# Performance work log

Hardware: AMD Instinct MI355X
Metric: run time of the kernel (lower is better)

The kernel has to match this reference:

```python
import jax, jax.numpy as jnp
import numpy as np

DIM = 256
EPS = 1e-5

def setup_inputs() -> dict:
    key = jax.random.key(0)
    ks = jax.random.split(key, 10)
    B, S, D = 8, 4096, DIM
    sc = 1.0 / np.sqrt(D)
    return {
        "supervised_embedding": jax.random.normal(ks[0], (B, S, D), jnp.float32),
        "transformer_embedding": jax.random.normal(ks[1], (B, S, D), jnp.float32),
        "Wq": jax.random.normal(ks[2], (D, D), jnp.float32) * sc,
        "bq": jnp.zeros((D,), jnp.float32),
        "Wk": jax.random.normal(ks[3], (D, D), jnp.float32) * sc,
        "bk": jnp.zeros((D,), jnp.float32),
        "Wv": jax.random.normal(ks[4], (D, D), jnp.float32) * sc,
        "bv": jnp.zeros((D,), jnp.float32),
        "gamma": jnp.ones((D,), jnp.float32),
        "beta": jnp.zeros((D,), jnp.float32),
    }

def _layernorm(x, gamma, beta):
    mu = jnp.mean(x, axis=-1, keepdims=True)
    var = jnp.mean(jnp.square(x - mu), axis=-1, keepdims=True)
    return (x - mu) * jax.lax.rsqrt(var + EPS) * gamma + beta

def reference(supervised_embedding, transformer_embedding, Wq, bq, Wk, bk, Wv, bv, gamma, beta):
    # torch Linear: y = x @ W.T + b
    q = transformer_embedding @ Wq.T + bq          # [B,S,D]
    k = supervised_embedding @ Wk.T + bk           # [B,S,D]
    v = supervised_embedding @ Wv.T + bv           # [B,S,D]
    scale = 1.0 / jnp.sqrt(jnp.asarray(q.shape[-1], q.dtype))
    scores = jnp.einsum('bqd,bkd->bqk', q, k) * scale  # [B,S,S]
    w = jax.nn.softmax(scores, axis=-1)
    combined = jnp.einsum('bqk,bkd->bqd', w, v)    # [B,S,D]
    out = _layernorm(combined + transformer_embedding, gamma, beta)
    return jnp.squeeze(out, axis=1) if out.shape[1] == 1 else out
```

## Files before the change

### kernel.cpp

```cpp
#include <hip/hip_runtime.h>
#include <hip/hip_bf16.h>

typedef short s16x8 __attribute__((ext_vector_type(8)));
typedef unsigned short u16x4 __attribute__((ext_vector_type(4)));
typedef float f32x4 __attribute__((ext_vector_type(4)));
typedef unsigned short u16;

#define DEV static __device__ __forceinline__

#if __has_builtin(__builtin_amdgcn_exp2f)
#define EXP2F(x) __builtin_amdgcn_exp2f(x)
#else
#define EXP2F(x) exp2f(x)
#endif

constexpr int D    = 256;
constexpr int SEQ  = 4096;
constexpr int NB   = 8;
constexpr int NTOK = NB * SEQ;
constexpr size_t N_EMB = (size_t)NTOK * D;
constexpr size_t N_W   = (size_t)D * D;
constexpr float SM_C = 0.09016844005556021f;
constexpr float SMAX = 128.0f;

DEV u16 f2bf(float f){ unsigned v; __builtin_memcpy(&v,&f,4); v += 0x7fffu + ((v>>16)&1u); return (u16)(v>>16); }

DEV float rsum16(float v){
  v += __shfl_xor(v,1); v += __shfl_xor(v,2);
  v += __shfl_xor(v,4); v += __shfl_xor(v,8);
  return v;
}

DEV void gl2lds16(const u16* g, void* lds){
  __builtin_amdgcn_global_load_lds(
      (const __attribute__((address_space(1))) void*)g,
      (__attribute__((address_space(3))) void*)lds, 16, 0, 0);
}
DEV void lgkm_barrier(){
  __builtin_amdgcn_s_waitcnt(0xC07F);
  __builtin_amdgcn_s_barrier();
}

__global__ __launch_bounds__(256)
void cvt_all(const float* __restrict__ TE, const float* __restrict__ SE,
             const float* __restrict__ Wq, const float* __restrict__ Wk,
             const float* __restrict__ Wv, u16* __restrict__ dst)
{
  const size_t total4 = (2*N_EMB + 3*N_W) / 4;
  for (size_t i = (size_t)blockIdx.x*256 + threadIdx.x; i < total4;
       i += (size_t)gridDim.x*256) {
    size_t e = i*4;
    const float* s;
    if      (e < N_EMB)            s = TE + e;
    else if (e < 2*N_EMB)          s = SE + (e - N_EMB);
    else if (e < 2*N_EMB + N_W)    s = Wq + (e - 2*N_EMB);
    else if (e < 2*N_EMB + 2*N_W)  s = Wk + (e - 2*N_EMB - N_W);
    else                           s = Wv + (e - 2*N_EMB - 2*N_W);
    f32x4 v = *(const f32x4*)s;
    u16x4 o;
#pragma unroll
    for (int j = 0; j < 4; j++) o[j] = f2bf(v[j]);
    *(u16x4*)(dst + e) = o;
  }
}

__global__ __launch_bounds__(256, 3)
void qkv_proj(const u16* __restrict__ TEb, const u16* __restrict__ SEb,
              const u16* __restrict__ Wqb, const float* __restrict__ bq,
              const u16* __restrict__ Wkb, const float* __restrict__ bk,
              const u16* __restrict__ Wvb, const float* __restrict__ bv,
              u16* __restrict__ Qb, u16* __restrict__ Kb, u16* __restrict__ Vt)
{
  __shared__ __align__(16) char wlds[32768];
  const int tid  = threadIdx.x;
  const int lane = tid & 63, wv = tid >> 6;
  const int li   = lane & 15, grp = lane >> 4;
  const int mode  = blockIdx.y >> 2;
  const int strip = blockIdx.y & 3;
  const int o0    = strip * 64;
  const int tbase = blockIdx.x * 512;

  const u16*   X    = (mode == 0) ? TEb : SEb;
  const u16*   W    = (mode == 0) ? Wqb : (mode == 1) ? Wkb : Wvb;
  const float* bias = (mode == 0) ? bq  : (mode == 1) ? bk  : bv;

#pragma unroll
  for (int c = 0; c < 8; c++) {
    int g = tid + 256*c;
    int r = g >> 5, jj = g & 31;
    *(s16x8*)(wlds + r*512 + 16*(jj ^ (r & 7))) =
        *(const s16x8*)(W + (size_t)(o0 + r)*D + jj*8);
  }
  __syncthreads();

#pragma unroll 1
  for (int tt = 0; tt < 2; tt++) {
    const int base = tbase + tt*256 + wv*64;
    f32x4 acc[16];
#pragma unroll
    for (int i = 0; i < 16; i++) acc[i] = (f32x4){0.f,0.f,0.f,0.f};

    if (mode < 2) {
#pragma unroll
      for (int ks = 0; ks < 8; ks++) {
        s16x8 a[4], bw[4];
#pragma unroll
        for (int mt = 0; mt < 4; mt++)
          a[mt] = *(const s16x8*)(X + (size_t)(base + 16*mt + li)*D + ks*32 + grp*8);
#pragma unroll
        for (int nt = 0; nt < 4; nt++) {
          int r = 16*nt + li;
          bw[nt] = *(const s16x8*)(wlds + r*512 + 16*((4*ks + grp) ^ (r & 7)));
        }
#pragma unroll
        for (int mt = 0; mt < 4; mt++)
#pragma unroll
          for (int nt = 0; nt < 4; nt++)
            acc[mt*4+nt] = __builtin_amdgcn_mfma_f32_16x16x32_bf16(a[mt], bw[nt], acc[mt*4+nt], 0,0,0);
      }
      u16* Y = (mode == 0) ? Qb : Kb;
#pragma unroll
      for (int nt = 0; nt < 4; nt++) {
        int col = o0 + 16*nt + li;
        float bb = bias[col];
#pragma unroll
        for (int mt = 0; mt < 4; mt++)
#pragma unroll
          for (int r = 0; r < 4; r++)
            Y[(size_t)(base + 16*mt + grp*4 + r)*D + col] = f2bf(acc[mt*4+nt][r] + bb);
      }
    } else {
#pragma unroll
      for (int ks = 0; ks < 8; ks++) {
        s16x8 aw[4], bx[4];
#pragma unroll
        for (int at = 0; at < 4; at++) {
          int r = 16*at + li;
          aw[at] = *(const s16x8*)(wlds + r*512 + 16*((4*ks + grp) ^ (r & 7)));
        }
#pragma unroll
        for (int bt = 0; bt < 4; bt++)
          bx[bt] = *(const s16x8*)(X + (size_t)(base + 16*bt + li)*D + ks*32 + grp*8);
#pragma unroll
        for (int at = 0; at < 4; at++)
#pragma unroll
          for (int bt = 0; bt < 4; bt++)
            acc[at*4+bt] = __builtin_amdgcn_mfma_f32_16x16x32_bf16(aw[at], bx[bt], acc[at*4+bt], 0,0,0);
      }
      const int b = base >> 12, s0 = base & (SEQ - 1);
#pragma unroll
      for (int at = 0; at < 4; at++) {
#pragma unroll
        for (int r = 0; r < 4; r++) {
          int o = o0 + 16*at + grp*4 + r;
          float bb = bias[o];
          u16* yrow = Vt + ((size_t)b*D + o)*SEQ + s0;
#pragma unroll
          for (int bt = 0; bt < 4; bt++)
            yrow[16*bt + li] = f2bf(acc[at*4+bt][r] + bb);
        }
      }
    }
  }
}

constexpr int KB0   = 0;
constexpr int KB1   = 16384;
constexpr int P_OFF = 32768;
constexpr int PSTR  = 36;
constexpr int L_OFF = 37376;
constexpr int G_OFF = 37632;
constexpr int BE_OFF= 38656;
constexpr int LDS_SZ= 39680;
constexpr int NIT   = SEQ / 32;

__global__ __launch_bounds__(256, 3)
void attn_ln(const u16* __restrict__ Qb, const u16* __restrict__ Kb,
             const u16* __restrict__ Vt, const float* __restrict__ TE,
             const float* __restrict__ gamma, const float* __restrict__ beta,
             float* __restrict__ out)
{
  __shared__ __align__(16) char smem[LDS_SZ];
  const int tid  = threadIdx.x;
  const int lane = tid & 63, wv = tid >> 6;
  const int li   = lane & 15, grp = lane >> 4;
  const int b  = blockIdx.x & 7;
  const int q0 = (blockIdx.x >> 3) * 64;

  float* gam = (float*)(smem + G_OFF);
  float* bet = (float*)(smem + BE_OFF);
  gam[tid] = gamma[tid];
  bet[tid] = beta[tid];

  const u16* Kbase = Kb + (size_t)b * SEQ * D;
  const u16* Vbase = Vt + (size_t)b * D * SEQ;

  const u16* qrow = Qb + ((size_t)b*SEQ + q0 + 16*wv + li)*D + grp*8;
  s16x8 qf[8];
#pragma unroll
  for (int ks = 0; ks < 8; ks++) qf[ks] = *(const s16x8*)(qrow + ks*32);

  int soff[4];
#pragma unroll
  for (int c = 0; c < 4; c++) {
    int u = wv*4 + c;
    int r = 2*u + (lane >> 5);
    soff[c] = r*256 + (((lane & 31) ^ (r & 7)) * 8);
  }
  int voff[4];
#pragma unroll
  for (int nt = 0; nt < 4; nt++) voff[nt] = (64*wv + 16*nt + li)*SEQ + grp*8;

#pragma unroll
  for (int c = 0; c < 4; c++)
    gl2lds16(Kbase + soff[c], smem + KB0 + (wv*4 + c)*1024);

  f32x4 oacc[16];
#pragma unroll
  for (int i = 0; i < 16; i++) oacc[i] = (f32x4){0.f,0.f,0.f,0.f};
  float l_r[4] = {0.f,0.f,0.f,0.f};

  u16* Pl = (u16*)(smem + P_OFF);

  for (int it = 0; it < NIT; it++) {
    const int k0 = it * 32;
    __syncthreads();

    {
      const u16* Kt = Kbase + (size_t)((it+1 < NIT) ? (k0+32) : k0) * D;
      char* kbn = smem + ((it & 1) ? KB0 : KB1);
#pragma unroll
      for (int c = 0; c < 4; c++)
        gl2lds16(Kt + soff[c], kbn + (wv*4 + c)*1024);
    }
    s16x8 vf[4];
#pragma unroll
    for (int nt = 0; nt < 4; nt++)
      vf[nt] = *(const s16x8*)(Vbase + voff[nt] + k0);

    const char* kb = smem + ((it & 1) ? KB1 : KB0);
    f32x4 sa0 = {0.f,0.f,0.f,0.f}, sa1 = {0.f,0.f,0.f,0.f};
    {
      const int r0 = li, r1 = li + 16;
      const char* kp0 = kb + r0*512;
      const char* kp1 = kb + r1*512;
#pragma unroll
      for (int ks = 0; ks < 8; ks++) {
        s16x8 k0f = *(const s16x8*)(kp0 + 16*((4*ks + grp) ^ (r0 & 7)));
        sa0 = __builtin_amdgcn_mfma_f32_16x16x32_bf16(qf[ks], k0f, sa0, 0,0,0);
        s16x8 k1f = *(const s16x8*)(kp1 + 16*((4*ks + grp) ^ (r1 & 7)));
        sa1 = __builtin_amdgcn_mfma_f32_16x16x32_bf16(qf[ks], k1f, sa1, 0,0,0);
      }
    }

#pragma unroll
    for (int r = 0; r < 4; r++) {
      float p0 = EXP2F((sa0[r] - SMAX) * SM_C);
      float p1 = EXP2F((sa1[r] - SMAX) * SM_C);
      l_r[r] += p0 + p1;
      int row = 16*wv + grp*4 + r;
      Pl[row*PSTR + li]      = f2bf(p0);
      Pl[row*PSTR + li + 16] = f2bf(p1);
    }
    lgkm_barrier();

#pragma unroll
    for (int mt = 0; mt < 4; mt++) {
      s16x8 pf = *(const s16x8*)(smem + P_OFF + ((16*mt + li)*PSTR + grp*8)*2);
#pragma unroll
      for (int nt = 0; nt < 4; nt++)
        oacc[mt*4+nt] = __builtin_amdgcn_mfma_f32_16x16x32_bf16(pf, vf[nt], oacc[mt*4+nt], 0,0,0);
    }
  }

  float* l_lds = (float*)(smem + L_OFF);
  {
#pragma unroll
    for (int r = 0; r < 4; r++) {
      float lt = rsum16(l_r[r]);
      if (li == 0) l_lds[16*wv + grp*4 + r] = lt;
    }
  }
  __syncthreads();

  const float* Tg = TE + ((size_t)b*SEQ + q0) * D;
  float s1[4][4], s2[4][4];
#pragma unroll
  for (int mt = 0; mt < 4; mt++) {
#pragma unroll
    for (int r = 0; r < 4; r++) {
      int row = 16*mt + grp*4 + r;
      float linv = 1.0f / l_lds[row];
      float ps = 0.f, pq = 0.f;
#pragma unroll
      for (int nt = 0; nt < 4; nt++) {
        int d_ = 64*wv + 16*nt + li;
        float x = oacc[mt*4+nt][r] * linv + Tg[(size_t)row*D + d_];
        oacc[mt*4+nt][r] = x;
        ps += x; pq += x * x;
      }
      s1[mt][r] = rsum16(ps);
      s2[mt][r] = rsum16(pq);
    }
  }
  float* part1 = (float*)(smem + P_OFF);
  float* part2 = (float*)(smem + P_OFF + 1024);
  if (li == 0) {
#pragma unroll
    for (int mt = 0; mt < 4; mt++)
#pragma unroll
      for (int r = 0; r < 4; r++) {
        int row = 16*mt + grp*4 + r;
        part1[row*4 + wv] = s1[mt][r];
        part2[row*4 + wv] = s2[mt][r];
      }
  }
  __syncthreads();
#pragma unroll
  for (int mt = 0; mt < 4; mt++) {
#pragma unroll
    for (int r = 0; r < 4; r++) {
      int row = 16*mt + grp*4 + r;
      float su = part1[row*4+0] + part1[row*4+1] + part1[row*4+2] + part1[row*4+3];
      float sq = part2[row*4+0] + part2[row*4+1] + part2[row*4+2] + part2[row*4+3];
      float mu  = su * (1.0f/256.0f);
      float var = sq * (1.0f/256.0f) - mu*mu;
      float rstd = rsqrtf(var + 1e-5f);
      float* orow = out + ((size_t)b*SEQ + q0 + row) * D;
#pragma unroll
      for (int nt = 0; nt < 4; nt++) {
        int d_ = 64*wv + 16*nt + li;
        orow[d_] = (oacc[mt*4+nt][r] - mu) * rstd * gam[d_] + bet[d_];
      }
    }
  }
}

extern "C" void kernel_launch(void* const* d_in, const int* in_sizes, int n_in,
                              void* d_out, int out_size, void* d_ws, size_t ws_size,
                              hipStream_t stream)
{
  (void)in_sizes; (void)n_in; (void)out_size; (void)ws_size;
  const float* SE = (const float*)d_in[0];
  const float* TE = (const float*)d_in[1];
  const float* Wq = (const float*)d_in[2];
  const float* bq = (const float*)d_in[3];
  const float* Wk = (const float*)d_in[4];
  const float* bk = (const float*)d_in[5];
  const float* Wv = (const float*)d_in[6];
  const float* bv = (const float*)d_in[7];
  const float* gm = (const float*)d_in[8];
  const float* bt = (const float*)d_in[9];

  u16* Qb  = (u16*)d_ws;
  u16* Kb  = Qb + N_EMB;
  u16* Vtr = Kb + N_EMB;
  u16* CVT = Vtr + N_EMB;
  u16* TEb = CVT;
  u16* SEb = TEb + N_EMB;
  u16* Wqb = SEb + N_EMB;
  u16* Wkb = Wqb + N_W;
  u16* Wvb = Wkb + N_W;

  cvt_all<<<2048, 256, 0, stream>>>(TE, SE, Wq, Wk, Wv, CVT);
  qkv_proj<<<dim3(NTOK/512, 12), 256, 0, stream>>>(TEb, SEb, Wqb, bq, Wkb, bk, Wvb, bv, Qb, Kb, Vtr);
  attn_ln<<<dim3((SEQ/64) * NB), 256, 0, stream>>>(Qb, Kb, Vtr, TE, gm, bt, (float*)d_out);
}
```

Baseline: 340.1 us.

## Split attention over key halves and combine with a separate layernorm kernel

```diff
diff --git a/kernel.cpp b/kernel.cpp
--- a/kernel.cpp
+++ b/kernel.cpp
@@ -23,6 +23,7 @@
 constexpr float SM_C = 0.09016844005556021f;
 constexpr float SMAX = 128.0f;
 
+DEV float bf2f(u16 u){ unsigned v = ((unsigned)u) << 16; float f; __builtin_memcpy(&f,&v,4); return f; }
 DEV u16 f2bf(float f){ unsigned v; __builtin_memcpy(&v,&f,4); v += 0x7fffu + ((v>>16)&1u); return (u16)(v>>16); }
 
 DEV float rsum16(float v){
@@ -64,7 +65,7 @@
   }
 }
 
-__global__ __launch_bounds__(256, 3)
+__global__ __launch_bounds__(256, 2)
 void qkv_proj(const u16* __restrict__ TEb, const u16* __restrict__ SEb,
               const u16* __restrict__ Wqb, const float* __restrict__ bq,
               const u16* __restrict__ Wkb, const float* __restrict__ bk,
@@ -100,13 +101,27 @@
 #pragma unroll
     for (int i = 0; i < 16; i++) acc[i] = (f32x4){0.f,0.f,0.f,0.f};
 
+    const u16* xr[4];
+#pragma unroll
+    for (int mt = 0; mt < 4; mt++)
+      xr[mt] = X + (size_t)(base + 16*mt + li)*D + grp*8;
+
+    s16x8 xa[4], xb[4];
+#pragma unroll
+    for (int mt = 0; mt < 4; mt++) xa[mt] = *(const s16x8*)(xr[mt]);
+
     if (mode < 2) {
+      u16* Y = (mode == 0) ? Qb : Kb;
 #pragma unroll
       for (int ks = 0; ks < 8; ks++) {
-        s16x8 a[4], bw[4];
-#pragma unroll
-        for (int mt = 0; mt < 4; mt++)
-          a[mt] = *(const s16x8*)(X + (size_t)(base + 16*mt + li)*D + ks*32 + grp*8);
+        s16x8* cu = (ks & 1) ? xb : xa;
+        s16x8* nx = (ks & 1) ? xa : xb;
+        if (ks < 7) {
+#pragma unroll
+          for (int mt = 0; mt < 4; mt++)
+            nx[mt] = *(const s16x8*)(xr[mt] + (ks+1)*32);
+        }
+        s16x8 bw[4];
 #pragma unroll
         for (int nt = 0; nt < 4; nt++) {
           int r = 16*nt + li;
@@ -116,9 +131,8 @@
         for (int mt = 0; mt < 4; mt++)
 #pragma unroll
           for (int nt = 0; nt < 4; nt++)
-            acc[mt*4+nt] = __builtin_amdgcn_mfma_f32_16x16x32_bf16(a[mt], bw[nt], acc[mt*4+nt], 0,0,0);
-      }
-      u16* Y = (mode == 0) ? Qb : Kb;
+            acc[mt*4+nt] = __builtin_amdgcn_mfma_f32_16x16x32_bf16(cu[mt], bw[nt], acc[mt*4+nt], 0,0,0);
+      }
 #pragma unroll
       for (int nt = 0; nt < 4; nt++) {
         int col = o0 + 16*nt + li;
@@ -132,20 +146,24 @@
     } else {
 #pragma unroll
       for (int ks = 0; ks < 8; ks++) {
-        s16x8 aw[4], bx[4];
+        s16x8* cu = (ks & 1) ? xb : xa;
+        s16x8* nx = (ks & 1) ? xa : xb;
+        if (ks < 7) {
+#pragma unroll
+          for (int bt = 0; bt < 4; bt++)
+            nx[bt] = *(const s16x8*)(xr[bt] + (ks+1)*32);
+        }
+        s16x8 aw[4];
 #pragma unroll
         for (int at = 0; at < 4; at++) {
           int r = 16*at + li;
           aw[at] = *(const s16x8*)(wlds + r*512 + 16*((4*ks + grp) ^ (r & 7)));
         }
 #pragma unroll
-        for (int bt = 0; bt < 4; bt++)
-          bx[bt] = *(const s16x8*)(X + (size_t)(base + 16*bt + li)*D + ks*32 + grp*8);
-#pragma unroll
         for (int at = 0; at < 4; at++)
 #pragma unroll
           for (int bt = 0; bt < 4; bt++)
-            acc[at*4+bt] = __builtin_amdgcn_mfma_f32_16x16x32_bf16(aw[at], bx[bt], acc[at*4+bt], 0,0,0);
+            acc[at*4+bt] = __builtin_amdgcn_mfma_f32_16x16x32_bf16(aw[at], cu[bt], acc[at*4+bt], 0,0,0);
       }
       const int b = base >> 12, s0 = base & (SEQ - 1);
 #pragma unroll
@@ -168,32 +186,25 @@
 constexpr int KB1   = 16384;
 constexpr int P_OFF = 32768;
 constexpr int PSTR  = 36;
-constexpr int L_OFF = 37376;
-constexpr int G_OFF = 37632;
-constexpr int BE_OFF= 38656;
-constexpr int LDS_SZ= 39680;
-constexpr int NIT   = SEQ / 32;
-
-__global__ __launch_bounds__(256, 3)
-void attn_ln(const u16* __restrict__ Qb, const u16* __restrict__ Kb,
-             const u16* __restrict__ Vt, const float* __restrict__ TE,
-             const float* __restrict__ gamma, const float* __restrict__ beta,
-             float* __restrict__ out)
-{
-  __shared__ __align__(16) char smem[LDS_SZ];
+constexpr int LDS_A = 37376;
+constexpr int NIT   = 64;
+
+__global__ __launch_bounds__(256, 2)
+void attn_fa(const u16* __restrict__ Qb, const u16* __restrict__ Kb,
+             const u16* __restrict__ Vt,
+             u16* __restrict__ O0, u16* __restrict__ O1, float* __restrict__ lsum)
+{
+  __shared__ __align__(16) char smem[LDS_A];
   const int tid  = threadIdx.x;
   const int lane = tid & 63, wv = tid >> 6;
   const int li   = lane & 15, grp = lane >> 4;
   const int b  = blockIdx.x & 7;
-  const int q0 = (blockIdx.x >> 3) * 64;
-
-  float* gam = (float*)(smem + G_OFF);
-  float* bet = (float*)(smem + BE_OFF);
-  gam[tid] = gamma[tid];
-  bet[tid] = beta[tid];
-
-  const u16* Kbase = Kb + (size_t)b * SEQ * D;
-  const u16* Vbase = Vt + (size_t)b * D * SEQ;
+  const int h  = (blockIdx.x >> 3) & 1;
+  const int q0 = (blockIdx.x >> 4) * 64;
+  u16* Op = h ? O1 : O0;
+
+  const u16* Kbase = Kb + ((size_t)b*SEQ + h*2048) * D;
+  const u16* Vbase = Vt + (size_t)b * D * SEQ + h*2048;
 
   const u16* qrow = Qb + ((size_t)b*SEQ + q0 + 16*wv + li)*D + grp*8;
   s16x8 qf[8];
@@ -273,66 +284,56 @@
     }
   }
 
-  float* l_lds = (float*)(smem + L_OFF);
-  {
+#pragma unroll
+  for (int mt = 0; mt < 4; mt++) {
 #pragma unroll
     for (int r = 0; r < 4; r++) {
-      float lt = rsum16(l_r[r]);
-      if (li == 0) l_lds[16*wv + grp*4 + r] = lt;
-    }
-  }
-  __syncthreads();
-
-  const float* Tg = TE + ((size_t)b*SEQ + q0) * D;
-  float s1[4][4], s2[4][4];
-#pragma unroll
-  for (int mt = 0; mt < 4; mt++) {
-#pragma unroll
-    for (int r = 0; r < 4; r++) {
-      int row = 16*mt + grp*4 + r;
-      float linv = 1.0f / l_lds[row];
-      float ps = 0.f, pq = 0.f;
-#pragma unroll
-      for (int nt = 0; nt < 4; nt++) {
-        int d_ = 64*wv + 16*nt + li;
-        float x = oacc[mt*4+nt][r] * linv + Tg[(size_t)row*D + d_];
-        oacc[mt*4+nt][r] = x;
-        ps += x; pq += x * x;
-      }
-      s1[mt][r] = rsum16(ps);
-      s2[mt][r] = rsum16(pq);
-    }
-  }
-  float* part1 = (float*)(smem + P_OFF);
-  float* part2 = (float*)(smem + P_OFF + 1024);
-  if (li == 0) {
-#pragma unroll
-    for (int mt = 0; mt < 4; mt++)
-#pragma unroll
-      for (int r = 0; r < 4; r++) {
-        int row = 16*mt + grp*4 + r;
-        part1[row*4 + wv] = s1[mt][r];
-        part2[row*4 + wv] = s2[mt][r];
-      }
-  }
-  __syncthreads();
-#pragma unroll
-  for (int mt = 0; mt < 4; mt++) {
-#pragma unroll
-    for (int r = 0; r < 4; r++) {
-      int row = 16*mt + grp*4 + r;
-      float su = part1[row*4+0] + part1[row*4+1] + part1[row*4+2] + part1[row*4+3];
-      float sq = part2[row*4+0] + part2[row*4+1] + part2[row*4+2] + part2[row*4+3];
-      float mu  = su * (1.0f/256.0f);
-      float var = sq * (1.0f/256.0f) - mu*mu;
-      float rstd = rsqrtf(var + 1e-5f);
-      float* orow = out + ((size_t)b*SEQ + q0 + row) * D;
-#pragma unroll
-      for (int nt = 0; nt < 4; nt++) {
-        int d_ = 64*wv + 16*nt + li;
-        orow[d_] = (oacc[mt*4+nt][r] - mu) * rstd * gam[d_] + bet[d_];
-      }
-    }
+      size_t row = (size_t)b*SEQ + q0 + 16*mt + grp*4 + r;
+#pragma unroll
+      for (int nt = 0; nt < 4; nt++)
+        Op[row*D + 64*wv + 16*nt + li] = f2bf(oacc[mt*4+nt][r]);
+    }
+  }
+#pragma unroll
+  for (int r = 0; r < 4; r++) {
+    float lt = rsum16(l_r[r]);
+    if (li == 0)
+      lsum[(size_t)h*NTOK + (size_t)b*SEQ + q0 + 16*wv + grp*4 + r] = lt;
+  }
+}
+
+__global__ __launch_bounds__(256, 2)
+void combine_ln(const u16* __restrict__ O0, const u16* __restrict__ O1,
+                const float* __restrict__ lsum, const float* __restrict__ TE,
+                const float* __restrict__ gamma, const float* __restrict__ beta,
+                float* __restrict__ out)
+{
+  const int tid = threadIdx.x, lane = tid & 63, wv = tid >> 6;
+  const int base = blockIdx.x * 64 + wv * 16;
+  f32x4 g4 = *(const f32x4*)(gamma + lane*4);
+  f32x4 b4 = *(const f32x4*)(beta  + lane*4);
+#pragma unroll 1
+  for (int rr = 0; rr < 16; rr++) {
+    const size_t tok = (size_t)base + rr;
+    u16x4 a0 = *(const u16x4*)(O0 + tok*D + lane*4);
+    u16x4 a1 = *(const u16x4*)(O1 + tok*D + lane*4);
+    f32x4 te = *(const f32x4*)(TE + tok*D + lane*4);
+    float inv = 1.0f / (lsum[tok] + lsum[(size_t)NTOK + tok]);
+    f32x4 x; float ps = 0.f, pq = 0.f;
+#pragma unroll
+    for (int j = 0; j < 4; j++) {
+      x[j] = (bf2f(a0[j]) + bf2f(a1[j])) * inv + te[j];
+      ps += x[j]; pq += x[j]*x[j];
+    }
+#pragma unroll
+    for (int o = 1; o < 64; o <<= 1) { ps += __shfl_xor(ps, o); pq += __shfl_xor(pq, o); }
+    float mu = ps * (1.0f/256.0f);
+    float var = pq * (1.0f/256.0f) - mu*mu;
+    float rstd = rsqrtf(var + 1e-5f);
+    f32x4 y;
+#pragma unroll
+    for (int j = 0; j < 4; j++) y[j] = (x[j] - mu) * rstd * g4[j] + b4[j];
+    *(f32x4*)(out + tok*D + lane*4) = y;
   }
 }
 
@@ -361,8 +362,12 @@
   u16* Wqb = SEb + N_EMB;
   u16* Wkb = Wqb + N_W;
   u16* Wvb = Wkb + N_W;
+  u16*   O0p = TEb;
+  u16*   O1p = SEb;
+  float* lsum = (float*)Wqb;
 
   cvt_all<<<2048, 256, 0, stream>>>(TE, SE, Wq, Wk, Wv, CVT);
   qkv_proj<<<dim3(NTOK/512, 12), 256, 0, stream>>>(TEb, SEb, Wqb, bq, Wkb, bk, Wvb, bv, Qb, Kb, Vtr);
-  attn_ln<<<dim3((SEQ/64) * NB), 256, 0, stream>>>(Qb, Kb, Vtr, TE, gm, bt, (float*)d_out);
-}
+  attn_fa<<<dim3((SEQ/64) * NB * 2), 256, 0, stream>>>(Qb, Kb, Vtr, O0p, O1p, lsum);
+  combine_ln<<<dim3(NTOK/64), 256, 0, stream>>>(O0p, O1p, lsum, TE, gm, bt, (float*)d_out);
+}
```

After: 344.0 us. No clear change (+1.2%).

## Software-pipeline attention PV step and double-buffer X loads in projection

Applied to the files above, without the earlier changes.

```diff
diff --git a/kernel.cpp b/kernel.cpp
--- a/kernel.cpp
+++ b/kernel.cpp
@@ -64,7 +64,7 @@
   }
 }
 
-__global__ __launch_bounds__(256, 3)
+__global__ __launch_bounds__(256, 2)
 void qkv_proj(const u16* __restrict__ TEb, const u16* __restrict__ SEb,
               const u16* __restrict__ Wqb, const float* __restrict__ bq,
               const u16* __restrict__ Wkb, const float* __restrict__ bk,
@@ -100,13 +100,27 @@
 #pragma unroll
     for (int i = 0; i < 16; i++) acc[i] = (f32x4){0.f,0.f,0.f,0.f};
 
+    const u16* xr[4];
+#pragma unroll
+    for (int mt = 0; mt < 4; mt++)
+      xr[mt] = X + (size_t)(base + 16*mt + li)*D + grp*8;
+
+    s16x8 xa[4], xb[4];
+#pragma unroll
+    for (int mt = 0; mt < 4; mt++) xa[mt] = *(const s16x8*)(xr[mt]);
+
     if (mode < 2) {
+      u16* Y = (mode == 0) ? Qb : Kb;
 #pragma unroll
       for (int ks = 0; ks < 8; ks++) {
-        s16x8 a[4], bw[4];
-#pragma unroll
-        for (int mt = 0; mt < 4; mt++)
-          a[mt] = *(const s16x8*)(X + (size_t)(base + 16*mt + li)*D + ks*32 + grp*8);
+        s16x8* cu = (ks & 1) ? xb : xa;
+        s16x8* nx = (ks & 1) ? xa : xb;
+        if (ks < 7) {
+#pragma unroll
+          for (int mt = 0; mt < 4; mt++)
+            nx[mt] = *(const s16x8*)(xr[mt] + (ks+1)*32);
+        }
+        s16x8 bw[4];
 #pragma unroll
         for (int nt = 0; nt < 4; nt++) {
           int r = 16*nt + li;
@@ -116,9 +130,8 @@
         for (int mt = 0; mt < 4; mt++)
 #pragma unroll
           for (int nt = 0; nt < 4; nt++)
-            acc[mt*4+nt] = __builtin_amdgcn_mfma_f32_16x16x32_bf16(a[mt], bw[nt], acc[mt*4+nt], 0,0,0);
-      }
-      u16* Y = (mode == 0) ? Qb : Kb;
+            acc[mt*4+nt] = __builtin_amdgcn_mfma_f32_16x16x32_bf16(cu[mt], bw[nt], acc[mt*4+nt], 0,0,0);
+      }
 #pragma unroll
       for (int nt = 0; nt < 4; nt++) {
         int col = o0 + 16*nt + li;
@@ -132,20 +145,24 @@
     } else {
 #pragma unroll
       for (int ks = 0; ks < 8; ks++) {
-        s16x8 aw[4], bx[4];
+        s16x8* cu = (ks & 1) ? xb : xa;
+        s16x8* nx = (ks & 1) ? xa : xb;
+        if (ks < 7) {
+#pragma unroll
+          for (int bt = 0; bt < 4; bt++)
+            nx[bt] = *(const s16x8*)(xr[bt] + (ks+1)*32);
+        }
+        s16x8 aw[4];
 #pragma unroll
         for (int at = 0; at < 4; at++) {
           int r = 16*at + li;
           aw[at] = *(const s16x8*)(wlds + r*512 + 16*((4*ks + grp) ^ (r & 7)));
         }
 #pragma unroll
-        for (int bt = 0; bt < 4; bt++)
-          bx[bt] = *(const s16x8*)(X + (size_t)(base + 16*bt + li)*D + ks*32 + grp*8);
-#pragma unroll
         for (int at = 0; at < 4; at++)
 #pragma unroll
           for (int bt = 0; bt < 4; bt++)
-            acc[at*4+bt] = __builtin_amdgcn_mfma_f32_16x16x32_bf16(aw[at], bx[bt], acc[at*4+bt], 0,0,0);
+            acc[at*4+bt] = __builtin_amdgcn_mfma_f32_16x16x32_bf16(aw[at], cu[bt], acc[at*4+bt], 0,0,0);
       }
       const int b = base >> 12, s0 = base & (SEQ - 1);
 #pragma unroll
@@ -174,7 +191,7 @@
 constexpr int LDS_SZ= 39680;
 constexpr int NIT   = SEQ / 32;
 
-__global__ __launch_bounds__(256, 3)
+__global__ __launch_bounds__(256, 2)
 void attn_ln(const u16* __restrict__ Qb, const u16* __restrict__ Kb,
              const u16* __restrict__ Vt, const float* __restrict__ TE,
              const float* __restrict__ gamma, const float* __restrict__ beta,
@@ -222,28 +239,27 @@
 
   u16* Pl = (u16*)(smem + P_OFF);
 
-  for (int it = 0; it < NIT; it++) {
+  s16x8 vfA[4], vfB[4];
+
+  auto body = [&](int it, char* kbc, char* kbn, s16x8* vcur, s16x8* vnxt) {
     const int k0 = it * 32;
     __syncthreads();
 
     {
       const u16* Kt = Kbase + (size_t)((it+1 < NIT) ? (k0+32) : k0) * D;
-      char* kbn = smem + ((it & 1) ? KB0 : KB1);
 #pragma unroll
       for (int c = 0; c < 4; c++)
         gl2lds16(Kt + soff[c], kbn + (wv*4 + c)*1024);
     }
-    s16x8 vf[4];
 #pragma unroll
     for (int nt = 0; nt < 4; nt++)
-      vf[nt] = *(const s16x8*)(Vbase + voff[nt] + k0);
-
-    const char* kb = smem + ((it & 1) ? KB1 : KB0);
+      vnxt[nt] = *(const s16x8*)(Vbase + voff[nt] + k0);
+
     f32x4 sa0 = {0.f,0.f,0.f,0.f}, sa1 = {0.f,0.f,0.f,0.f};
     {
       const int r0 = li, r1 = li + 16;
-      const char* kp0 = kb + r0*512;
-      const char* kp1 = kb + r1*512;
+      const char* kp0 = kbc + r0*512;
+      const char* kp1 = kbc + r1*512;
 #pragma unroll
       for (int ks = 0; ks < 8; ks++) {
         s16x8 k0f = *(const s16x8*)(kp0 + 16*((4*ks + grp) ^ (r0 & 7)));
@@ -252,6 +268,17 @@
         sa1 = __builtin_amdgcn_mfma_f32_16x16x32_bf16(qf[ks], k1f, sa1, 0,0,0);
       }
     }
+
+    if (it > 0) {
+#pragma unroll
+      for (int mt = 0; mt < 4; mt++) {
+        s16x8 pf = *(const s16x8*)(smem + P_OFF + ((16*mt + li)*PSTR + grp*8)*2);
+#pragma unroll
+        for (int nt = 0; nt < 4; nt++)
+          oacc[mt*4+nt] = __builtin_amdgcn_mfma_f32_16x16x32_bf16(pf, vcur[nt], oacc[mt*4+nt], 0,0,0);
+      }
+    }
+    lgkm_barrier();
 
 #pragma unroll
     for (int r = 0; r < 4; r++) {
@@ -262,15 +289,21 @@
       Pl[row*PSTR + li]      = f2bf(p0);
       Pl[row*PSTR + li + 16] = f2bf(p1);
     }
-    lgkm_barrier();
-
-#pragma unroll
-    for (int mt = 0; mt < 4; mt++) {
-      s16x8 pf = *(const s16x8*)(smem + P_OFF + ((16*mt + li)*PSTR + grp*8)*2);
-#pragma unroll
-      for (int nt = 0; nt < 4; nt++)
-        oacc[mt*4+nt] = __builtin_amdgcn_mfma_f32_16x16x32_bf16(pf, vf[nt], oacc[mt*4+nt], 0,0,0);
-    }
+  };
+
+#pragma unroll 1
+  for (int it = 0; it < NIT; it += 2) {
+    body(it,     smem + KB0, smem + KB1, vfA, vfB);
+    body(it + 1, smem + KB1, smem + KB0, vfB, vfA);
+  }
+
+  __syncthreads();
+#pragma unroll
+  for (int mt = 0; mt < 4; mt++) {
+    s16x8 pf = *(const s16x8*)(smem + P_OFF + ((16*mt + li)*PSTR + grp*8)*2);
+#pragma unroll
+    for (int nt = 0; nt < 4; nt++)
+      oacc[mt*4+nt] = __builtin_amdgcn_mfma_f32_16x16x32_bf16(pf, vfA[nt], oacc[mt*4+nt], 0,0,0);
   }
 
   float* l_lds = (float*)(smem + L_OFF);
```

After: 325.4 us. -4.3%, faster.
